# Optimization experiments

Measured on AMD Instinct MI355X. Metric: run time of the kernel, lower is better.

Reference implementation:

```python
import jax, jax.numpy as jnp
import numpy as np

BATCH, LENGTH, FEAT, RANK = 4096, 128, 4, 64
SCALE = 1.0 / np.sqrt(RANK)  # keep 128-step matrix chain numerically stable


def setup_inputs() -> dict:
    key = jax.random.key(0)
    k1, k2, k3, k4 = jax.random.split(key, 4)
    return {
        "input_data": jax.random.normal(k1, (BATCH, LENGTH, FEAT), dtype=jnp.float32),
        "first_core": jax.random.normal(k2, (FEAT, RANK), dtype=jnp.float32) * SCALE,
        "mid_cores": jax.random.normal(k3, (LENGTH - 2, RANK, FEAT, RANK), dtype=jnp.float32) * SCALE,
        "last_core": jax.random.normal(k4, (RANK, FEAT), dtype=jnp.float32) * SCALE,
    }


def reference(input_data, first_core, mid_cores, last_core):
    # input_data: [b, L, f] -> site-major [L, b, f]
    x = jnp.transpose(input_data, (1, 0, 2))
    # Per-site contraction with the physical (feature) index.
    v0 = jnp.einsum("ir,bi->br", first_core, x[0])            # [b, r]
    mid_mats = jnp.einsum("slir,sbi->sblr", mid_cores, x[1:-1])  # [S, b, r, r]
    last_vec = jnp.einsum("li,bi->bl", last_core, x[-1])      # [b, r]

    # Sequential tensor-train chain: v <- v @ M_s for each middle site.
    def step(v, mat):
        return jnp.einsum("bl,blr->br", v, mat), None

    v, _ = jax.lax.scan(step, v0, mid_mats)
    # Final contraction against last site vector -> [b, 1]
    out = jnp.sum(v * last_vec, axis=-1, keepdims=True)
    return out
```

## Files before the change

kernel.cpp:

```cpp
#include <hip/hip_runtime.h>
#include <hip/hip_fp16.h>
#include <stdint.h>

#define NSITES 126
#define XPITCH 516
#define VPITCH 68

typedef _Float16 half8_t  __attribute__((ext_vector_type(8)));
typedef float    float4_t __attribute__((ext_vector_type(4)));

#define LBAR() asm volatile("s_waitcnt lgkmcnt(0)\n\ts_barrier" ::: "memory")

__global__ __launch_bounds__(256) void repack_g(const float* __restrict__ mid,
                                                _Float16* __restrict__ gt) {
    __shared__ float lds[64 * 260];
    const int s = blockIdx.x;
    const int t = threadIdx.x;
    const float* src = mid + (size_t)s * 16384;
#pragma unroll
    for (int k = 0; k < 16; ++k) {
        const int f4 = t + 256 * k;
        const int l = f4 >> 6, n0 = (f4 & 63) * 4;
        *(float4_t*)&lds[l * 260 + n0] = *(const float4_t*)&src[f4 * 4];
    }
    __syncthreads();
    half8_t* dst = (half8_t*)gt + (size_t)s * 2048;
#pragma unroll
    for (int m = 0; m < 8; ++m) {
        const int F = t + 256 * m;
        const int lane = F & 63, w = (F >> 6) & 3, h = (F >> 8) & 1, i = F >> 9;
        const int q = lane >> 4, c = lane & 15;
        const int n = i * 64 + w * 16 + c;
        half8_t o;
#pragma unroll
        for (int j = 0; j < 8; ++j)
            o[j] = (_Float16)lds[(32 * h + 8 * q + j) * 260 + n];
        dst[F] = o;
    }
}

__global__ __launch_bounds__(256) void tt_chain(
    const float* __restrict__ x,
    const float* __restrict__ first,
    const float* __restrict__ last,
    const _Float16* __restrict__ gt,
    float* __restrict__ out) {

    __shared__ float vbuf[2][16 * VPITCH];
    __shared__ float xbuf[16 * XPITCH];
    __shared__ int   eacc[16];

    const int tid  = threadIdx.x;
    const int w    = tid >> 6;
    const int lane = tid & 63;
    const int q    = lane >> 4;
    const int c    = lane & 15;
    const int b0   = blockIdx.x * 16;

    {
        const int bb = tid >> 4, seg = tid & 15;
        const float4_t* src = (const float4_t*)(x + (size_t)(b0 + bb) * 512 + seg * 32);
        float4_t* dst = (float4_t*)(xbuf + bb * XPITCH + seg * 32);
#pragma unroll
        for (int k = 0; k < 8; ++k) dst[k] = src[k];
    }
    if (tid < 16) eacc[tid] = 0;
    __syncthreads();

    {
        const int bb = tid >> 4, rq = tid & 15;
        const float xs0 = xbuf[bb * XPITCH + 0], xs1 = xbuf[bb * XPITCH + 1];
        const float xs2 = xbuf[bb * XPITCH + 2], xs3 = xbuf[bb * XPITCH + 3];
#pragma unroll
        for (int k = 0; k < 4; ++k) {
            const int r = rq * 4 + k;
            vbuf[0][bb * VPITCH + r] =
                xs0 * first[r] + xs1 * first[64 + r] + xs2 * first[128 + r] + xs3 * first[192 + r];
        }
    }

    half8_t F0[8], F1[8], F2[8];
    const half8_t* gb = (const half8_t*)gt + w * 64 + lane;
    auto LOAD = [&](int s, half8_t* F) {
        const half8_t* p = gb + (size_t)s * 2048;
#pragma unroll
        for (int ih = 0; ih < 8; ++ih) F[ih] = p[ih * 256];
    };
    LOAD(0, F0);
    LOAD(1, F1);
    LBAR();

    auto STEP = [&](int s, half8_t* F) {
        const int p = s & 1;
        const float* vr = &vbuf[p][c * VPITCH];
        float4_t a0lo = *(const float4_t*)(vr + q * 8);
        float4_t a0hi = *(const float4_t*)(vr + q * 8 + 4);
        float4_t a1lo = *(const float4_t*)(vr + 32 + q * 8);
        float4_t a1hi = *(const float4_t*)(vr + 32 + q * 8 + 4);

        if ((s & 7) == 0 && s != 0) {
            float m = 0.f;
#pragma unroll
            for (int k = 0; k < 4; ++k) {
                m = fmaxf(m, fabsf(a0lo[k])); m = fmaxf(m, fabsf(a0hi[k]));
                m = fmaxf(m, fabsf(a1lo[k])); m = fmaxf(m, fabsf(a1hi[k]));
            }
            m = fmaxf(m, __shfl_xor(m, 16));
            m = fmaxf(m, __shfl_xor(m, 32));
            int e = 0;
            if (m > 0.f) frexpf(m, &e);
            const float sc = ldexpf(1.0f, -e);
#pragma unroll
            for (int k = 0; k < 4; ++k) {
                a0lo[k] *= sc; a0hi[k] *= sc; a1lo[k] *= sc; a1hi[k] *= sc;
            }
            if (tid < 16) eacc[tid] += e;
        }

        half8_t af0, af1;
#pragma unroll
        for (int k = 0; k < 4; ++k) {
            af0[k] = (_Float16)a0lo[k]; af0[4 + k] = (_Float16)a0hi[k];
            af1[k] = (_Float16)a1lo[k]; af1[4 + k] = (_Float16)a1hi[k];
        }

        float4_t xs[4];
#pragma unroll
        for (int jj = 0; jj < 4; ++jj)
            xs[jj] = *(const float4_t*)(xbuf + (q * 4 + jj) * XPITCH + (s + 1) * 4);

        float4_t acc[4];
#pragma unroll
        for (int i = 0; i < 4; ++i) {
            float4_t z = {0.f, 0.f, 0.f, 0.f};
            z = __builtin_amdgcn_mfma_f32_16x16x32_f16(af0, F[i * 2 + 0], z, 0, 0, 0);
            z = __builtin_amdgcn_mfma_f32_16x16x32_f16(af1, F[i * 2 + 1], z, 0, 0, 0);
            acc[i] = z;
        }

#pragma unroll
        for (int jj = 0; jj < 4; ++jj) {
            const float vn = xs[jj].x * acc[0][jj] + xs[jj].y * acc[1][jj] +
                             xs[jj].z * acc[2][jj] + xs[jj].w * acc[3][jj];
            vbuf[p ^ 1][(q * 4 + jj) * VPITCH + w * 16 + c] = vn;
        }
        LBAR();
    };

    for (int s = 0; s < NSITES; s += 3) {
        const int s2 = (s + 2 < NSITES) ? s + 2 : NSITES - 1;
        const int s3 = (s + 3 < NSITES) ? s + 3 : NSITES - 1;
        const int s4 = (s + 4 < NSITES) ? s + 4 : NSITES - 1;
        LOAD(s2, F2);
        STEP(s, F0);
        LOAD(s3, F0);
        STEP(s + 1, F1);
        LOAD(s4, F1);
        STEP(s + 2, F2);
    }

    {
        const int bb = tid >> 4, rq = tid & 15;
        const float x0 = xbuf[bb * XPITCH + 508], x1 = xbuf[bb * XPITCH + 509];
        const float x2 = xbuf[bb * XPITCH + 510], x3 = xbuf[bb * XPITCH + 511];
        float dot = 0.f;
#pragma unroll
        for (int k = 0; k < 4; ++k) {
            const int r = rq * 4 + k;
            const float lv = last[r * 4 + 0] * x0 + last[r * 4 + 1] * x1 +
                             last[r * 4 + 2] * x2 + last[r * 4 + 3] * x3;
            dot += lv * vbuf[0][bb * VPITCH + r];
        }
#pragma unroll
        for (int o = 8; o > 0; o >>= 1) dot += __shfl_xor(dot, o, 16);
        if (rq == 0) out[b0 + bb] = ldexpf(dot, eacc[bb]);
    }
}

extern "C" void kernel_launch(void* const* d_in, const int* in_sizes, int n_in,
                              void* d_out, int out_size, void* d_ws, size_t ws_size,
                              hipStream_t stream) {
    (void)in_sizes; (void)n_in; (void)out_size; (void)ws_size;
    const float* x     = (const float*)d_in[0];
    const float* first = (const float*)d_in[1];
    const float* mid   = (const float*)d_in[2];
    const float* last  = (const float*)d_in[3];
    float* out = (float*)d_out;
    _Float16* gt = (_Float16*)d_ws;

    repack_g<<<126, 256, 0, stream>>>(mid, gt);
    tt_chain<<<256, 256, 0, stream>>>(x, first, last, gt, out);
}
```

Before: 124.4 us.

## Keep tensor-train state in registers with single-wave blocks and permuted core layout

Restructures the chain kernel so each single-wave block processes 32 batch rows and keeps the state vector in MFMA operand registers across steps. The repack permutes core columns so the MFMA output layout directly feeds the next step, removing the per-step LDS exchange and barriers. The whole per-site core slice is held in registers with double buffering. This trades away parallelism (fewer, larger waves) and raises register pressure for a shorter per-step dependency path.

```diff
diff --git a/kernel.cpp b/kernel.cpp
--- a/kernel.cpp
+++ b/kernel.cpp
@@ -4,18 +4,18 @@
 
 #define NSITES 126
 #define XPITCH 516
-#define VPITCH 68
 
 typedef _Float16 half8_t  __attribute__((ext_vector_type(8)));
 typedef float    float4_t __attribute__((ext_vector_type(4)));
 
-#define LBAR() asm volatile("s_waitcnt lgkmcnt(0)\n\ts_barrier" ::: "memory")
+__device__ __forceinline__ constexpr int rho_map(int u, int m) {
+    return 32*(u>>1) + 8*(m>>2) + 4*(u&1) + (m&3);
+}
 
 __global__ __launch_bounds__(256) void repack_g(const float* __restrict__ mid,
                                                 _Float16* __restrict__ gt) {
     __shared__ float lds[64 * 260];
-    const int s = blockIdx.x;
-    const int t = threadIdx.x;
+    const int s = blockIdx.x, t = threadIdx.x;
     const float* src = mid + (size_t)s * 16384;
 #pragma unroll
     for (int k = 0; k < 16; ++k) {
@@ -28,152 +28,172 @@
 #pragma unroll
     for (int m = 0; m < 8; ++m) {
         const int F = t + 256 * m;
-        const int lane = F & 63, w = (F >> 6) & 3, h = (F >> 8) & 1, i = F >> 9;
+        const int lane = F & 63, fi = F >> 6;
+        const int kk = fi >> 4, u = (fi >> 2) & 3, i = fi & 3;
         const int q = lane >> 4, c = lane & 15;
-        const int n = i * 64 + w * 16 + c;
+        const int n = 64 * i + rho_map(u, c);
         half8_t o;
 #pragma unroll
         for (int j = 0; j < 8; ++j)
-            o[j] = (_Float16)lds[(32 * h + 8 * q + j) * 260 + n];
+            o[j] = (_Float16)lds[(32 * kk + 8 * q + j) * 260 + n];
         dst[F] = o;
     }
 }
 
-__global__ __launch_bounds__(256) void tt_chain(
+__global__ __launch_bounds__(64, 1) void tt_chain(
     const float* __restrict__ x,
     const float* __restrict__ first,
     const float* __restrict__ last,
     const _Float16* __restrict__ gt,
     float* __restrict__ out) {
 
-    __shared__ float vbuf[2][16 * VPITCH];
-    __shared__ float xbuf[16 * XPITCH];
-    __shared__ int   eacc[16];
-
-    const int tid  = threadIdx.x;
-    const int w    = tid >> 6;
-    const int lane = tid & 63;
-    const int q    = lane >> 4;
-    const int c    = lane & 15;
-    const int b0   = blockIdx.x * 16;
+    __shared__ float xbuf[32 * XPITCH];
+    const int lane = threadIdx.x;
+    const int q = lane >> 4, c = lane & 15;
+    const int b0 = blockIdx.x * 32;
 
     {
-        const int bb = tid >> 4, seg = tid & 15;
-        const float4_t* src = (const float4_t*)(x + (size_t)(b0 + bb) * 512 + seg * 32);
-        float4_t* dst = (float4_t*)(xbuf + bb * XPITCH + seg * 32);
-#pragma unroll
-        for (int k = 0; k < 8; ++k) dst[k] = src[k];
-    }
-    if (tid < 16) eacc[tid] = 0;
+        const float4_t* src = (const float4_t*)(x + (size_t)b0 * 512);
+#pragma unroll
+        for (int k = 0; k < 64; ++k) {
+            const int f4 = lane + 64 * k;
+            const int row = f4 >> 7, col4 = f4 & 127;
+            *(float4_t*)&xbuf[row * XPITCH + col4 * 4] = src[f4];
+        }
+    }
     __syncthreads();
 
+    half8_t FA[32], FB[32];
+    auto LOAD = [&](int s, half8_t* F) {
+        const half8_t* p = (const half8_t*)gt + (size_t)s * 2048 + lane;
+#pragma unroll
+        for (int fi = 0; fi < 32; ++fi) F[fi] = p[fi * 64];
+    };
+    LOAD(0, FA);
+    LOAD(1, FB);
+
+    half8_t bf[2][2];
     {
-        const int bb = tid >> 4, rq = tid & 15;
-        const float xs0 = xbuf[bb * XPITCH + 0], xs1 = xbuf[bb * XPITCH + 1];
-        const float xs2 = xbuf[bb * XPITCH + 2], xs3 = xbuf[bb * XPITCH + 3];
-#pragma unroll
-        for (int k = 0; k < 4; ++k) {
-            const int r = rq * 4 + k;
-            vbuf[0][bb * VPITCH + r] =
-                xs0 * first[r] + xs1 * first[64 + r] + xs2 * first[128 + r] + xs3 * first[192 + r];
-        }
-    }
-
-    half8_t F0[8], F1[8], F2[8];
-    const half8_t* gb = (const half8_t*)gt + w * 64 + lane;
-    auto LOAD = [&](int s, half8_t* F) {
-        const half8_t* p = gb + (size_t)s * 2048;
-#pragma unroll
-        for (int ih = 0; ih < 8; ++ih) F[ih] = p[ih * 256];
+        float4_t xs0[2];
+        xs0[0] = *(const float4_t*)&xbuf[c * XPITCH];
+        xs0[1] = *(const float4_t*)&xbuf[(c + 16) * XPITCH];
+#pragma unroll
+        for (int kk = 0; kk < 2; ++kk) {
+            float4_t vlo[2] = {{0,0,0,0},{0,0,0,0}};
+            float4_t vhi[2] = {{0,0,0,0},{0,0,0,0}};
+#pragma unroll
+            for (int i = 0; i < 4; ++i) {
+                const float4_t flo = *(const float4_t*)&first[i*64 + 32*kk + 8*q];
+                const float4_t fhi = *(const float4_t*)&first[i*64 + 32*kk + 8*q + 4];
+#pragma unroll
+                for (int g = 0; g < 2; ++g) {
+                    const float xv = xs0[g][i];
+                    const float4_t xv4 = {xv, xv, xv, xv};
+                    vlo[g] = __builtin_elementwise_fma(flo, xv4, vlo[g]);
+                    vhi[g] = __builtin_elementwise_fma(fhi, xv4, vhi[g]);
+                }
+            }
+#pragma unroll
+            for (int g = 0; g < 2; ++g) {
+                half8_t nb;
+#pragma unroll
+                for (int jj = 0; jj < 4; ++jj) {
+                    nb[jj]     = (_Float16)vlo[g][jj];
+                    nb[4 + jj] = (_Float16)vhi[g][jj];
+                }
+                bf[g][kk] = nb;
+            }
+        }
+    }
+
+    float4_t comb[2][4];
+    int e0 = 0, e1 = 0;
+
+    auto STEP = [&](int s, half8_t* F) {
+        float4_t xs[2];
+        xs[0] = *(const float4_t*)&xbuf[c * XPITCH + 4 * (s + 1)];
+        xs[1] = *(const float4_t*)&xbuf[(c + 16) * XPITCH + 4 * (s + 1)];
+#pragma unroll
+        for (int g = 0; g < 2; ++g)
+#pragma unroll
+            for (int u = 0; u < 4; ++u) {
+                float4_t cc = {0, 0, 0, 0};
+#pragma unroll
+                for (int i = 0; i < 4; ++i) {
+                    float4_t z = {0, 0, 0, 0};
+                    z = __builtin_amdgcn_mfma_f32_16x16x32_f16(F[u*4 + i],      bf[g][0], z, 0, 0, 0);
+                    z = __builtin_amdgcn_mfma_f32_16x16x32_f16(F[16 + u*4 + i], bf[g][1], z, 0, 0, 0);
+                    const float xv = xs[g][i];
+                    const float4_t xv4 = {xv, xv, xv, xv};
+                    cc = __builtin_elementwise_fma(z, xv4, cc);
+                }
+                comb[g][u] = cc;
+            }
+
+        if (((s + 1) & 7) == 0) {
+            float m0 = 0.f, m1 = 0.f;
+#pragma unroll
+            for (int u = 0; u < 4; ++u)
+#pragma unroll
+                for (int jj = 0; jj < 4; ++jj) {
+                    m0 = fmaxf(m0, fabsf(comb[0][u][jj]));
+                    m1 = fmaxf(m1, fabsf(comb[1][u][jj]));
+                }
+            m0 = fmaxf(m0, __shfl_xor(m0, 16)); m0 = fmaxf(m0, __shfl_xor(m0, 32));
+            m1 = fmaxf(m1, __shfl_xor(m1, 16)); m1 = fmaxf(m1, __shfl_xor(m1, 32));
+            int ee0 = 0, ee1 = 0;
+            if (m0 > 0.f) frexpf(m0, &ee0);
+            if (m1 > 0.f) frexpf(m1, &ee1);
+            const float sc0 = ldexpf(1.f, -ee0), sc1 = ldexpf(1.f, -ee1);
+#pragma unroll
+            for (int u = 0; u < 4; ++u) {
+                comb[0][u] *= sc0;
+                comb[1][u] *= sc1;
+            }
+            e0 += ee0; e1 += ee1;
+        }
+
+#pragma unroll
+        for (int g = 0; g < 2; ++g) {
+            half8_t n0, n1;
+#pragma unroll
+            for (int jj = 0; jj < 4; ++jj) {
+                n0[jj]     = (_Float16)comb[g][0][jj];
+                n0[4 + jj] = (_Float16)comb[g][1][jj];
+                n1[jj]     = (_Float16)comb[g][2][jj];
+                n1[4 + jj] = (_Float16)comb[g][3][jj];
+            }
+            bf[g][0] = n0;
+            bf[g][1] = n1;
+        }
     };
-    LOAD(0, F0);
-    LOAD(1, F1);
-    LBAR();
-
-    auto STEP = [&](int s, half8_t* F) {
-        const int p = s & 1;
-        const float* vr = &vbuf[p][c * VPITCH];
-        float4_t a0lo = *(const float4_t*)(vr + q * 8);
-        float4_t a0hi = *(const float4_t*)(vr + q * 8 + 4);
-        float4_t a1lo = *(const float4_t*)(vr + 32 + q * 8);
-        float4_t a1hi = *(const float4_t*)(vr + 32 + q * 8 + 4);
-
-        if ((s & 7) == 0 && s != 0) {
-            float m = 0.f;
-#pragma unroll
-            for (int k = 0; k < 4; ++k) {
-                m = fmaxf(m, fabsf(a0lo[k])); m = fmaxf(m, fabsf(a0hi[k]));
-                m = fmaxf(m, fabsf(a1lo[k])); m = fmaxf(m, fabsf(a1hi[k]));
-            }
-            m = fmaxf(m, __shfl_xor(m, 16));
-            m = fmaxf(m, __shfl_xor(m, 32));
-            int e = 0;
-            if (m > 0.f) frexpf(m, &e);
-            const float sc = ldexpf(1.0f, -e);
-#pragma unroll
-            for (int k = 0; k < 4; ++k) {
-                a0lo[k] *= sc; a0hi[k] *= sc; a1lo[k] *= sc; a1hi[k] *= sc;
-            }
-            if (tid < 16) eacc[tid] += e;
-        }
-
-        half8_t af0, af1;
-#pragma unroll
-        for (int k = 0; k < 4; ++k) {
-            af0[k] = (_Float16)a0lo[k]; af0[4 + k] = (_Float16)a0hi[k];
-            af1[k] = (_Float16)a1lo[k]; af1[4 + k] = (_Float16)a1hi[k];
-        }
-
-        float4_t xs[4];
-#pragma unroll
-        for (int jj = 0; jj < 4; ++jj)
-            xs[jj] = *(const float4_t*)(xbuf + (q * 4 + jj) * XPITCH + (s + 1) * 4);
-
-        float4_t acc[4];
-#pragma unroll
-        for (int i = 0; i < 4; ++i) {
-            float4_t z = {0.f, 0.f, 0.f, 0.f};
-            z = __builtin_amdgcn_mfma_f32_16x16x32_f16(af0, F[i * 2 + 0], z, 0, 0, 0);
-            z = __builtin_amdgcn_mfma_f32_16x16x32_f16(af1, F[i * 2 + 1], z, 0, 0, 0);
-            acc[i] = z;
-        }
-
-#pragma unroll
-        for (int jj = 0; jj < 4; ++jj) {
-            const float vn = xs[jj].x * acc[0][jj] + xs[jj].y * acc[1][jj] +
-                             xs[jj].z * acc[2][jj] + xs[jj].w * acc[3][jj];
-            vbuf[p ^ 1][(q * 4 + jj) * VPITCH + w * 16 + c] = vn;
-        }
-        LBAR();
-    };
-
-    for (int s = 0; s < NSITES; s += 3) {
-        const int s2 = (s + 2 < NSITES) ? s + 2 : NSITES - 1;
-        const int s3 = (s + 3 < NSITES) ? s + 3 : NSITES - 1;
-        const int s4 = (s + 4 < NSITES) ? s + 4 : NSITES - 1;
-        LOAD(s2, F2);
-        STEP(s, F0);
-        LOAD(s3, F0);
-        STEP(s + 1, F1);
-        LOAD(s4, F1);
-        STEP(s + 2, F2);
+
+    for (int s = 0; s < NSITES; s += 2) {
+        STEP(s, FA);
+        LOAD(s + 2 <= NSITES - 1 ? s + 2 : NSITES - 1, FA);
+        STEP(s + 1, FB);
+        LOAD(s + 3 <= NSITES - 1 ? s + 3 : NSITES - 1, FB);
     }
 
     {
-        const int bb = tid >> 4, rq = tid & 15;
-        const float x0 = xbuf[bb * XPITCH + 508], x1 = xbuf[bb * XPITCH + 509];
-        const float x2 = xbuf[bb * XPITCH + 510], x3 = xbuf[bb * XPITCH + 511];
-        float dot = 0.f;
-#pragma unroll
-        for (int k = 0; k < 4; ++k) {
-            const int r = rq * 4 + k;
-            const float lv = last[r * 4 + 0] * x0 + last[r * 4 + 1] * x1 +
-                             last[r * 4 + 2] * x2 + last[r * 4 + 3] * x3;
-            dot += lv * vbuf[0][bb * VPITCH + r];
-        }
-#pragma unroll
-        for (int o = 8; o > 0; o >>= 1) dot += __shfl_xor(dot, o, 16);
-        if (rq == 0) out[b0 + bb] = ldexpf(dot, eacc[bb]);
+        const float4_t xl0 = *(const float4_t*)&xbuf[c * XPITCH + 508];
+        const float4_t xl1 = *(const float4_t*)&xbuf[(c + 16) * XPITCH + 508];
+        float dot0 = 0.f, dot1 = 0.f;
+#pragma unroll
+        for (int u = 0; u < 4; ++u)
+#pragma unroll
+            for (int jj = 0; jj < 4; ++jj) {
+                const int r = rho_map(u, 4 * q + jj);
+                const float4_t lr = *(const float4_t*)&last[r * 4];
+                const float lv0 = lr[0]*xl0[0] + lr[1]*xl0[1] + lr[2]*xl0[2] + lr[3]*xl0[3];
+                const float lv1 = lr[0]*xl1[0] + lr[1]*xl1[1] + lr[2]*xl1[2] + lr[3]*xl1[3];
+                dot0 += comb[0][u][jj] * lv0;
+                dot1 += comb[1][u][jj] * lv1;
+            }
+        dot0 += __shfl_xor(dot0, 16); dot0 += __shfl_xor(dot0, 32);
+        dot1 += __shfl_xor(dot1, 16); dot1 += __shfl_xor(dot1, 32);
+        if (lane < 16)      out[b0 + lane] = ldexpf(dot0, e0);
+        else if (lane < 32) out[b0 + lane] = ldexpf(dot1, e1);
     }
 }
 
@@ -189,5 +209,5 @@
     _Float16* gt = (_Float16*)d_ws;
 
     repack_g<<<126, 256, 0, stream>>>(mid, gt);
-    tt_chain<<<256, 256, 0, stream>>>(x, first, last, gt, out);
-}
+    tt_chain<<<128, 64, 0, stream>>>(x, first, last, gt, out);
+}
```

Result: slower. 242.4 us (+94.9%).

## Run the chain in a single wave per block with register-resident state and no barriers

Applied to the files above, without the earlier changes.

Each 16-row batch tile now runs in one 64-lane wavefront instead of four. The chain vector stays in MFMA accumulator registers, with a permuted rank mapping (rho_map) in the repacked weights, so the per-step LDS round trip and block barriers go away. The x feature is folded into the B operand before the MFMA, and weight loads use inline asm with explicit vmcnt waits to pipeline per-quarter units. The risk is 4x fewer waves per block: each wave now does four times the serial MFMA work, which gives less latency hiding across 256 blocks. Note that p[(s&7)==0] normalisation semantics also shifted.

```diff
diff --git a/kernel.cpp b/kernel.cpp
--- a/kernel.cpp
+++ b/kernel.cpp
@@ -3,19 +3,30 @@
 #include <stdint.h>
 
 #define NSITES 126
-#define XPITCH 516
-#define VPITCH 68
+#define NUNITS (NSITES * 4)
+#define XP 516
 
 typedef _Float16 half8_t  __attribute__((ext_vector_type(8)));
+typedef _Float16 half4_t  __attribute__((ext_vector_type(4)));
 typedef float    float4_t __attribute__((ext_vector_type(4)));
 
-#define LBAR() asm volatile("s_waitcnt lgkmcnt(0)\n\ts_barrier" ::: "memory")
+#define WAITV(N) asm volatile("s_waitcnt vmcnt(" #N ")" ::: "memory")
+#define TIE8(P) asm volatile("" : "+v"((P)[0]), "+v"((P)[1]), "+v"((P)[2]), "+v"((P)[3]), \
+                                  "+v"((P)[4]), "+v"((P)[5]), "+v"((P)[6]), "+v"((P)[7]))
+
+__device__ __forceinline__ constexpr int rho_map(int u, int m) {
+    return 32*(u>>1) + 8*(m>>2) + 4*(u&1) + (m&3);
+}
+
+__device__ __forceinline__ void aload(half8_t& d, uint32_t voff, uint64_t sbase) {
+    asm volatile("global_load_dwordx4 %0, %1, %2 offset:0"
+                 : "=v"(d) : "v"(voff), "s"(sbase));
+}
 
 __global__ __launch_bounds__(256) void repack_g(const float* __restrict__ mid,
                                                 _Float16* __restrict__ gt) {
     __shared__ float lds[64 * 260];
-    const int s = blockIdx.x;
-    const int t = threadIdx.x;
+    const int s = blockIdx.x, t = threadIdx.x;
     const float* src = mid + (size_t)s * 16384;
 #pragma unroll
     for (int k = 0; k < 16; ++k) {
@@ -28,9 +39,10 @@
 #pragma unroll
     for (int m = 0; m < 8; ++m) {
         const int F = t + 256 * m;
-        const int lane = F & 63, w = (F >> 6) & 3, h = (F >> 8) & 1, i = F >> 9;
+        const int lane = F & 63, f = F >> 6;
+        const int u = f >> 3, i = (f >> 1) & 3, h = f & 1;
         const int q = lane >> 4, c = lane & 15;
-        const int n = i * 64 + w * 16 + c;
+        const int n = 64 * i + rho_map(u, c);
         half8_t o;
 #pragma unroll
         for (int j = 0; j < 8; ++j)
@@ -39,141 +51,150 @@
     }
 }
 
-__global__ __launch_bounds__(256) void tt_chain(
+__global__ __launch_bounds__(64, 1) void tt_chain(
     const float* __restrict__ x,
     const float* __restrict__ first,
     const float* __restrict__ last,
     const _Float16* __restrict__ gt,
     float* __restrict__ out) {
 
-    __shared__ float vbuf[2][16 * VPITCH];
-    __shared__ float xbuf[16 * XPITCH];
-    __shared__ int   eacc[16];
-
-    const int tid  = threadIdx.x;
-    const int w    = tid >> 6;
-    const int lane = tid & 63;
-    const int q    = lane >> 4;
-    const int c    = lane & 15;
-    const int b0   = blockIdx.x * 16;
+    __shared__ _Float16 xh[16 * XP];
+
+    const int lane = threadIdx.x;
+    const int q = lane >> 4, c = lane & 15;
+    const int b0 = blockIdx.x * 16;
 
     {
-        const int bb = tid >> 4, seg = tid & 15;
-        const float4_t* src = (const float4_t*)(x + (size_t)(b0 + bb) * 512 + seg * 32);
-        float4_t* dst = (float4_t*)(xbuf + bb * XPITCH + seg * 32);
-#pragma unroll
-        for (int k = 0; k < 8; ++k) dst[k] = src[k];
-    }
-    if (tid < 16) eacc[tid] = 0;
-    __syncthreads();
-
+        const float4_t* src = (const float4_t*)(x + (size_t)b0 * 512);
+#pragma unroll
+        for (int t = 0; t < 32; ++t) {
+            const int idx = lane + 64 * t;
+            const int bb = idx >> 7, col = idx & 127;
+            const float4_t v = src[idx];
+            half4_t hv = { (_Float16)v.x, (_Float16)v.y,
+                           (_Float16)v.z, (_Float16)v.w };
+            *(half4_t*)&xh[bb * XP + col * 4] = hv;
+        }
+    }
+
+    float4_t accv0, accv1, accv2, accv3;
     {
-        const int bb = tid >> 4, rq = tid & 15;
-        const float xs0 = xbuf[bb * XPITCH + 0], xs1 = xbuf[bb * XPITCH + 1];
-        const float xs2 = xbuf[bb * XPITCH + 2], xs3 = xbuf[bb * XPITCH + 3];
-#pragma unroll
-        for (int k = 0; k < 4; ++k) {
-            const int r = rq * 4 + k;
-            vbuf[0][bb * VPITCH + r] =
-                xs0 * first[r] + xs1 * first[64 + r] + xs2 * first[128 + r] + xs3 * first[192 + r];
-        }
+        const float* xr = x + (size_t)(b0 + c) * 512;
+        const float xi0 = xr[0], xi1 = xr[1], xi2 = xr[2], xi3 = xr[3];
+        float4_t* avp[4] = { &accv0, &accv1, &accv2, &accv3 };
+#pragma unroll
+        for (int u = 0; u < 4; ++u)
+#pragma unroll
+            for (int jj = 0; jj < 4; ++jj) {
+                const int r = rho_map(u, 4 * q + jj);
+                (*avp[u])[jj] = xi0 * first[r] + xi1 * first[64 + r] +
+                                xi2 * first[128 + r] + xi3 * first[192 + r];
+            }
     }
 
     half8_t F0[8], F1[8], F2[8];
-    const half8_t* gb = (const half8_t*)gt + w * 64 + lane;
-    auto LOAD = [&](int s, half8_t* F) {
-        const half8_t* p = gb + (size_t)s * 2048;
-#pragma unroll
-        for (int ih = 0; ih < 8; ++ih) F[ih] = p[ih * 256];
+    half8_t bf[8];
+    uint32_t voff[8];
+#pragma unroll
+    for (int k = 0; k < 8; ++k) voff[k] = k * 1024 + lane * 16;
+
+    auto LOADU = [&](int m, half8_t* F) {
+        const uint64_t sb = (uint64_t)gt + (uint32_t)m * 8192u;
+#pragma unroll
+        for (int k = 0; k < 8; ++k) aload(F[k], voff[k], sb);
     };
-    LOAD(0, F0);
-    LOAD(1, F1);
-    LBAR();
-
-    auto STEP = [&](int s, half8_t* F) {
-        const int p = s & 1;
-        const float* vr = &vbuf[p][c * VPITCH];
-        float4_t a0lo = *(const float4_t*)(vr + q * 8);
-        float4_t a0hi = *(const float4_t*)(vr + q * 8 + 4);
-        float4_t a1lo = *(const float4_t*)(vr + 32 + q * 8);
-        float4_t a1hi = *(const float4_t*)(vr + 32 + q * 8 + 4);
-
-        if ((s & 7) == 0 && s != 0) {
-            float m = 0.f;
-#pragma unroll
-            for (int k = 0; k < 4; ++k) {
-                m = fmaxf(m, fabsf(a0lo[k])); m = fmaxf(m, fabsf(a0hi[k]));
-                m = fmaxf(m, fabsf(a1lo[k])); m = fmaxf(m, fabsf(a1hi[k]));
+
+    int e0 = 0;
+    half4_t xnext = *(const half4_t*)&xh[c * XP + 1 * 4];
+
+    LOADU(0, F0);
+    LOADU(1, F1);
+
+#define MFMA_F16 __builtin_amdgcn_mfma_f32_16x16x32_f16
+#define UNIT(S, F, U, ACC) do {                                               \
+    WAITV(16);                                                                \
+    TIE8(F);                                                                  \
+    if ((U) == 0) {             \
+        const half4_t xcur = xnext;                                           \
+        const int sn_ = ((S) + 2 < 128) ? (S) + 2 : 127;                      \
+        xnext = *(const half4_t*)&xh[c * XP + sn_ * 4];                       \
+        half8_t vh0, vh1;                                                     \
+        _Pragma("unroll") for (int jj = 0; jj < 4; ++jj) {                    \
+            vh0[jj]     = (_Float16)accv0[jj];                                \
+            vh0[4 + jj] = (_Float16)accv1[jj];                                \
+            vh1[jj]     = (_Float16)accv2[jj];                                \
+            vh1[4 + jj] = (_Float16)accv3[jj];                                \
+        }                                                                     \
+        _Pragma("unroll") for (int i = 0; i < 4; ++i) {                       \
+            half8_t sp;                                                       \
+            _Pragma("unroll") for (int j = 0; j < 8; ++j) sp[j] = xcur[i];    \
+            bf[i * 2 + 0] = vh0 * sp;                                         \
+            bf[i * 2 + 1] = vh1 * sp;                                         \
+        }                                                                     \
+    }                                                                         \
+    {                                                                         \
+        float4_t a0_ = {0.f, 0.f, 0.f, 0.f}, a1_ = {0.f, 0.f, 0.f, 0.f};      \
+        a0_ = MFMA_F16((F)[0], bf[0], a0_, 0, 0, 0);                          \
+        a1_ = MFMA_F16((F)[1], bf[1], a1_, 0, 0, 0);                          \
+        a0_ = MFMA_F16((F)[2], bf[2], a0_, 0, 0, 0);                          \
+        a1_ = MFMA_F16((F)[3], bf[3], a1_, 0, 0, 0);                          \
+        a0_ = MFMA_F16((F)[4], bf[4], a0_, 0, 0, 0);                          \
+        a1_ = MFMA_F16((F)[5], bf[5], a1_, 0, 0, 0);                          \
+        a0_ = MFMA_F16((F)[6], bf[6], a0_, 0, 0, 0);                          \
+        a1_ = MFMA_F16((F)[7], bf[7], a1_, 0, 0, 0);                          \
+        ACC = a0_ + a1_;                                                      \
+    }                                                                         \
+    if ((U) == 3 && ((((S) + 1) & 7) == 0)) {      \
+        float m_ = 0.f;                                                       \
+        _Pragma("unroll") for (int jj = 0; jj < 4; ++jj) {                    \
+            m_ = fmaxf(m_, fabsf(accv0[jj])); m_ = fmaxf(m_, fabsf(accv1[jj]));\
+            m_ = fmaxf(m_, fabsf(accv2[jj])); m_ = fmaxf(m_, fabsf(accv3[jj]));\
+        }                                                                     \
+        m_ = fmaxf(m_, __shfl_xor(m_, 16));                                   \
+        m_ = fmaxf(m_, __shfl_xor(m_, 32));                                   \
+        int e_ = 0;                                                           \
+        if (m_ > 0.f) frexpf(m_, &e_);                                        \
+        const float sc_ = ldexpf(1.f, -e_);                                   \
+        accv0 *= sc_; accv1 *= sc_; accv2 *= sc_; accv3 *= sc_;               \
+        e0 += e_;                                                             \
+    }                                                                         \
+} while (0)
+
+    for (int t = 0; t < NUNITS; t += 12) {
+        const int s0 = t >> 2;
+        LOADU(t + 2,  F2);  UNIT(s0,     F0, 0, accv0);
+        LOADU(t + 3,  F0);  UNIT(s0,     F1, 1, accv1);
+        LOADU(t + 4,  F1);  UNIT(s0,     F2, 2, accv2);
+        LOADU(t + 5,  F2);  UNIT(s0,     F0, 3, accv3);
+        LOADU(t + 6,  F0);  UNIT(s0 + 1, F1, 0, accv0);
+        LOADU(t + 7,  F1);  UNIT(s0 + 1, F2, 1, accv1);
+        LOADU(t + 8,  F2);  UNIT(s0 + 1, F0, 2, accv2);
+        LOADU(t + 9,  F0);  UNIT(s0 + 1, F1, 3, accv3);
+        LOADU(t + 10, F1);  UNIT(s0 + 2, F2, 0, accv0);
+        LOADU(t + 11, F2);  UNIT(s0 + 2, F0, 1, accv1);
+        const int m1 = (t + 12 < NUNITS) ? t + 12 : NUNITS - 1;
+        const int m2 = (t + 13 < NUNITS) ? t + 13 : NUNITS - 1;
+        LOADU(m1, F0);      UNIT(s0 + 2, F1, 2, accv2);
+        LOADU(m2, F1);      UNIT(s0 + 2, F2, 3, accv3);
+    }
+    WAITV(0);
+
+    {
+        const float4_t xl = *(const float4_t*)(x + (size_t)(b0 + c) * 512 + 508);
+        const float4_t* avp[4] = { &accv0, &accv1, &accv2, &accv3 };
+        float dot = 0.f;
+#pragma unroll
+        for (int u = 0; u < 4; ++u)
+#pragma unroll
+            for (int jj = 0; jj < 4; ++jj) {
+                const int r = rho_map(u, 4 * q + jj);
+                const float4_t lr = *(const float4_t*)&last[r * 4];
+                dot += (*avp[u])[jj] *
+                       (lr[0] * xl[0] + lr[1] * xl[1] + lr[2] * xl[2] + lr[3] * xl[3]);
             }
-            m = fmaxf(m, __shfl_xor(m, 16));
-            m = fmaxf(m, __shfl_xor(m, 32));
-            int e = 0;
-            if (m > 0.f) frexpf(m, &e);
-            const float sc = ldexpf(1.0f, -e);
-#pragma unroll
-            for (int k = 0; k < 4; ++k) {
-                a0lo[k] *= sc; a0hi[k] *= sc; a1lo[k] *= sc; a1hi[k] *= sc;
-            }
-            if (tid < 16) eacc[tid] += e;
-        }
-
-        half8_t af0, af1;
-#pragma unroll
-        for (int k = 0; k < 4; ++k) {
-            af0[k] = (_Float16)a0lo[k]; af0[4 + k] = (_Float16)a0hi[k];
-            af1[k] = (_Float16)a1lo[k]; af1[4 + k] = (_Float16)a1hi[k];
-        }
-
-        float4_t xs[4];
-#pragma unroll
-        for (int jj = 0; jj < 4; ++jj)
-            xs[jj] = *(const float4_t*)(xbuf + (q * 4 + jj) * XPITCH + (s + 1) * 4);
-
-        float4_t acc[4];
-#pragma unroll
-        for (int i = 0; i < 4; ++i) {
-            float4_t z = {0.f, 0.f, 0.f, 0.f};
-            z = __builtin_amdgcn_mfma_f32_16x16x32_f16(af0, F[i * 2 + 0], z, 0, 0, 0);
-            z = __builtin_amdgcn_mfma_f32_16x16x32_f16(af1, F[i * 2 + 1], z, 0, 0, 0);
-            acc[i] = z;
-        }
-
-#pragma unroll
-        for (int jj = 0; jj < 4; ++jj) {
-            const float vn = xs[jj].x * acc[0][jj] + xs[jj].y * acc[1][jj] +
-                             xs[jj].z * acc[2][jj] + xs[jj].w * acc[3][jj];
-            vbuf[p ^ 1][(q * 4 + jj) * VPITCH + w * 16 + c] = vn;
-        }
-        LBAR();
-    };
-
-    for (int s = 0; s < NSITES; s += 3) {
-        const int s2 = (s + 2 < NSITES) ? s + 2 : NSITES - 1;
-        const int s3 = (s + 3 < NSITES) ? s + 3 : NSITES - 1;
-        const int s4 = (s + 4 < NSITES) ? s + 4 : NSITES - 1;
-        LOAD(s2, F2);
-        STEP(s, F0);
-        LOAD(s3, F0);
-        STEP(s + 1, F1);
-        LOAD(s4, F1);
-        STEP(s + 2, F2);
-    }
-
-    {
-        const int bb = tid >> 4, rq = tid & 15;
-        const float x0 = xbuf[bb * XPITCH + 508], x1 = xbuf[bb * XPITCH + 509];
-        const float x2 = xbuf[bb * XPITCH + 510], x3 = xbuf[bb * XPITCH + 511];
-        float dot = 0.f;
-#pragma unroll
-        for (int k = 0; k < 4; ++k) {
-            const int r = rq * 4 + k;
-            const float lv = last[r * 4 + 0] * x0 + last[r * 4 + 1] * x1 +
-                             last[r * 4 + 2] * x2 + last[r * 4 + 3] * x3;
-            dot += lv * vbuf[0][bb * VPITCH + r];
-        }
-#pragma unroll
-        for (int o = 8; o > 0; o >>= 1) dot += __shfl_xor(dot, o, 16);
-        if (rq == 0) out[b0 + bb] = ldexpf(dot, eacc[bb]);
+        dot += __shfl_xor(dot, 16);
+        dot += __shfl_xor(dot, 32);
+        if (lane < 16) out[b0 + lane] = ldexpf(dot, e0);
     }
 }
 
@@ -189,5 +210,5 @@
     _Float16* gt = (_Float16*)d_ws;
 
     repack_g<<<126, 256, 0, stream>>>(mid, gt);
-    tt_chain<<<256, 256, 0, stream>>>(x, first, last, gt, out);
-}
+    tt_chain<<<256, 64, 0, stream>>>(x, first, last, gt, out);
+}
```

Result: slower. 152.1 us (+22.2%).
